# Performance work log

Measured on AMD Instinct MI355X. Metric: run time of the kernel, lower is better.

## Reference

```python
import jax, jax.numpy as jnp
import numpy as np

NUM_LAYERS = 2


def setup_inputs() -> dict:
    key = jax.random.key(0)
    k1, k2, k3, k4 = jax.random.split(key, 4)
    N, E, D = 50000, 800000, 100
    features = jax.random.normal(k1, (N, D), dtype=jnp.float32)
    # stacked nn.Linear weights, one [D,D] per layer (no bias)
    W = jax.random.normal(k2, (NUM_LAYERS, D, D), dtype=jnp.float32) * 0.02
    src = jax.random.randint(k3, (E,), 0, N)
    dst = jax.random.randint(k4, (E,), 0, N)
    return {"features": features, "W": W, "src": src, "dst": dst}


def reference(features, W, src, dst):
    N, D = features.shape
    num_layers = W.shape[0]
    inv_lp1 = 1.0 / (num_layers + 1)

    # --- graph preprocessing (mirrors ItemConv.graph setter) ---
    # add self loops (fill_diag 1.0), then row-normalize by inverse degree
    loop = jnp.arange(N)
    src_all = jnp.concatenate([src, loop])  # message sources
    dst_all = jnp.concatenate([dst, loop])  # message destinations (rows of adj_t)
    deg = jax.ops.segment_sum(
        jnp.ones(src_all.shape, dtype=features.dtype), dst_all, num_segments=N
    )
    deg_inv = jnp.where(deg > 0, 1.0 / deg, 0.0)
    w = deg_inv[dst_all]  # per-edge weight: row-normalized, [E+N]

    # --- forward (LightGCN-style conv with linear projections) ---
    avg = features * inv_lp1
    x = features
    for i in range(num_layers):
        x = x @ W[i].T  # nn.Linear(D, D, bias=False)
        # SpMM: out[d] = sum_{e: dst=d} w_e * x[src_e]
        x = jax.ops.segment_sum(w[:, None] * x[src_all], dst_all, num_segments=N)
        # F.normalize(x): L2 along dim=-1 with eps=1e-12 (max-clamped norm)
        norm = jnp.linalg.norm(x, axis=-1, keepdims=True)
        avg = avg + (x / jnp.maximum(norm, 1e-12)) * inv_lp1
    return avg
```

## Files before the change

kernel.cpp:

```cpp
#include <hip/hip_runtime.h>

#define D 100
#define YSTRIDE 128
#define BSHIFT 7
#define BSIZE 128
#define BMASK 127
#define NBKMAX 512
#define EPB 2048
#define DCAP 4096

typedef __attribute__((ext_vector_type(8))) short bf8v;
typedef __attribute__((ext_vector_type(4))) float f4v;

__device__ inline unsigned short f2bf(float f) {
    unsigned u = __float_as_uint(f);
    return (unsigned short)((u + 0x7fffu + ((u >> 16) & 1u)) >> 16);
}
__device__ inline float bflo(unsigned v) { return __uint_as_float(v << 16); }
__device__ inline float bfhi(unsigned v) { return __uint_as_float(v & 0xffff0000u); }
__device__ inline unsigned short pk8(float a, float b) {
    return (unsigned short)(__builtin_amdgcn_cvt_pk_fp8_f32(a, b, 0, false) & 0xffff);
}
__device__ inline float up8lo(unsigned v) { return __builtin_amdgcn_cvt_f32_fp8((int)v, 0); }
__device__ inline float up8hi(unsigned v) { return __builtin_amdgcn_cvt_f32_fp8((int)v, 1); }

__device__ inline void acc8(float* acc, uint2 v, float w) {
    acc[0] = fmaf(__builtin_amdgcn_cvt_f32_fp8((int)v.x, 0), w, acc[0]);
    acc[1] = fmaf(__builtin_amdgcn_cvt_f32_fp8((int)v.x, 1), w, acc[1]);
    acc[2] = fmaf(__builtin_amdgcn_cvt_f32_fp8((int)v.x, 2), w, acc[2]);
    acc[3] = fmaf(__builtin_amdgcn_cvt_f32_fp8((int)v.x, 3), w, acc[3]);
    acc[4] = fmaf(__builtin_amdgcn_cvt_f32_fp8((int)v.y, 0), w, acc[4]);
    acc[5] = fmaf(__builtin_amdgcn_cvt_f32_fp8((int)v.y, 1), w, acc[5]);
    acc[6] = fmaf(__builtin_amdgcn_cvt_f32_fp8((int)v.y, 2), w, acc[6]);
    acc[7] = fmaf(__builtin_amdgcn_cvt_f32_fp8((int)v.y, 3), w, acc[7]);
}

__device__ inline void scan512_excl(int* a, int* t, int tid) {
    int v0 = a[2 * tid], v1 = a[2 * tid + 1];
    t[tid] = v0 + v1;
    __syncthreads();
    for (int off = 1; off < 256; off <<= 1) {
        int u = (tid >= off) ? t[tid - off] : 0;
        __syncthreads();
        t[tid] += u;
        __syncthreads();
    }
    int base = (tid ? t[tid - 1] : 0);
    a[2 * tid]     = base;
    a[2 * tid + 1] = base + v0;
    __syncthreads();
}

__global__ __launch_bounds__(256) void k_pre(const float* __restrict__ x0, const float* __restrict__ W,
                                             unsigned* __restrict__ s8, float* __restrict__ Wc,
                                             int* __restrict__ hist, const int* __restrict__ dst,
                                             int N, int E, int nbk, int packb, int ablk) {
    __shared__ int lhist[NBKMAX];
    int tid = threadIdx.x;
    int bx = blockIdx.x;

    if (bx < packb) {
        int t = bx * 256 + tid;
        if (t >= N * 32) return;
        int d = t >> 5, q = t & 31;
        unsigned p = 0u;
        if (q < D / 4) {
            float4 v = *(const float4*)(x0 + (long)d * D + q * 4);
            p = (unsigned)pk8(v.x, v.y) | ((unsigned)pk8(v.z, v.w) << 16);
        }
        s8[t] = p;
    } else if (bx < packb + ablk) {
        int blk = bx - packb;
        int base = blk * EPB;
        int count = min(EPB, E - base);
        for (int i = tid; i < NBKMAX; i += 256) lhist[i] = 0;
        __syncthreads();
        for (int i = tid; i < count; i += 256) atomicAdd(&lhist[dst[base + i] >> BSHIFT], 1);
        __syncthreads();
        for (int b = tid; b < NBKMAX; b += 256) hist[(long)blk * NBKMAX + b] = lhist[b];
    } else {
        int t = (bx - packb - ablk) * 256 + tid;
        if (t >= D * D) return;
        int i = t / D, j = t - i * D;
        const float* w2 = W + D * D + (long)i * D;
        float s = 0.f;
        for (int k = 0; k < D; k++) s += w2[k] * W[(long)k * D + j];
        Wc[t] = s;
    }
}

__global__ __launch_bounds__(256) void k_colscan_prep(const int* __restrict__ hist,
                                                      int* __restrict__ pref, int* __restrict__ bcnt,
                                                      int nebk, int nbk,
                                                      const float* __restrict__ W1,
                                                      const float* __restrict__ Wc,
                                                      unsigned short* __restrict__ P, int wtot) {
    int tid = threadIdx.x;
    if ((int)blockIdx.x < nbk) {
        int b = blockIdx.x;
        __shared__ int a[NBKMAX], t[256];
        int i0 = tid, i1 = tid + 256;
        a[i0] = (i0 < nebk) ? hist[(long)i0 * NBKMAX + b] : 0;
        a[i1] = (i1 < nebk) ? hist[(long)i1 * NBKMAX + b] : 0;
        __syncthreads();
        scan512_excl(a, t, tid);
        if (i0 < nebk) pref[(long)i0 * NBKMAX + b] = a[i0];
        if (i1 < nebk) pref[(long)i1 * NBKMAX + b] = a[i1];
        if (tid == 0) bcnt[b] = a[nebk];
    } else {
        int t2 = ((int)blockIdx.x - nbk) * 256 + tid;
        if (t2 >= wtot) return;
        int lane = t2 & 63;
        int r = t2 >> 6;
        int kt = r & 3;
        int r2 = r >> 2;
        int nt = r2 % 7;
        int l  = r2 / 7;
        const float* M = (l == 0) ? W1 : Wc;
        int ng = nt * 16 + (lane & 15);
        int k0 = kt * 32 + (lane >> 4) * 8;
        unsigned short u[8];
#pragma unroll
        for (int j = 0; j < 8; j++) {
            int k = k0 + j;
            u[j] = (ng < D && k < D) ? f2bf(M[(long)ng * D + k]) : (unsigned short)0;
        }
        uint4 o;
        o.x = (unsigned)u[0] | ((unsigned)u[1] << 16);
        o.y = (unsigned)u[2] | ((unsigned)u[3] << 16);
        o.z = (unsigned)u[4] | ((unsigned)u[5] << 16);
        o.w = (unsigned)u[6] | ((unsigned)u[7] << 16);
        *(uint4*)(P + (long)t2 * 8) = o;
    }
}

__global__ __launch_bounds__(256) void k_scanB(const int* __restrict__ bcnt,
                                               int* __restrict__ boff, int nbk, int E) {
    __shared__ int a[NBKMAX], t[256];
    int tid = threadIdx.x;
    a[tid]       = (tid < nbk) ? bcnt[tid] : 0;
    a[tid + 256] = (tid + 256 < nbk) ? bcnt[tid + 256] : 0;
    __syncthreads();
    scan512_excl(a, t, tid);
    if (tid < nbk)       boff[tid] = a[tid];
    if (tid + 256 < nbk) boff[tid + 256] = a[tid + 256];
    if (tid == 0) boff[nbk] = E;
}

__global__ __launch_bounds__(256) void k_bucketC(const int* __restrict__ src,
                                                 const int* __restrict__ dst,
                                                 const int* __restrict__ boff,
                                                 const int* __restrict__ pref,
                                                 unsigned* __restrict__ ebuf, int E, int nbk) {
    __shared__ int lhist[NBKMAX], lstart[NBKMAX], runS[NBKMAX], t[256];
    __shared__ unsigned stage[EPB];
    int tid = threadIdx.x;
    int base = blockIdx.x * EPB;
    int count = min(EPB, E - base);

    for (int i = tid; i < NBKMAX; i += 256) lhist[i] = 0;
    __syncthreads();
    for (int i = tid; i < count; i += 256) atomicAdd(&lhist[dst[base + i] >> BSHIFT], 1);
    __syncthreads();
    for (int i = tid; i < NBKMAX; i += 256) lstart[i] = lhist[i];
    __syncthreads();
    scan512_excl(lstart, t, tid);
    for (int b = tid; b < nbk; b += 256)
        runS[b] = boff[b] + pref[(long)blockIdx.x * NBKMAX + b];
    __syncthreads();
    for (int i = tid; i < NBKMAX; i += 256) lhist[i] = 0;
    __syncthreads();
    for (int i = tid; i < count; i += 256) {
        int dv = dst[base + i];
        int sv = src[base + i];
        int b = dv >> BSHIFT;
        int r = atomicAdd(&lhist[b], 1);
        stage[lstart[b] + r] = ((unsigned)(dv & BMASK) << 16) | (unsigned)sv;
    }
    __syncthreads();
    int wave = tid >> 6, lane = tid & 63;
    for (int b = wave; b < nbk; b += 4) {
        int c = lhist[b], ls = lstart[b], rs = runS[b];
        for (int j = lane; j < c; j += 64) ebuf[rs + j] = stage[ls + j];
    }
}

__global__ __launch_bounds__(256) void k_bucketD(const unsigned* __restrict__ ebuf,
                                                 const int* __restrict__ bucket_off,
                                                 int* __restrict__ col, int* __restrict__ rowptr,
                                                 int N, int nbk, int E) {
    __shared__ int lh[BSIZE], ls[BSIZE];
    __shared__ int colStage[DCAP];
    int b = blockIdx.x;
    int tid = threadIdx.x;
    int beg = bucket_off[b], end = bucket_off[b + 1];
    int cnt = end - beg;

    if (tid < BSIZE) lh[tid] = 0;
    __syncthreads();
    for (int i = tid; i < cnt; i += 256) atomicAdd(&lh[ebuf[beg + i] >> 16], 1);
    __syncthreads();
    if (tid < BSIZE) ls[tid] = lh[tid];
    __syncthreads();
    for (int off = 1; off < BSIZE; off <<= 1) {
        int v = (tid >= off && tid < BSIZE) ? ls[tid - off] : 0;
        __syncthreads();
        if (tid < BSIZE) ls[tid] += v;
        __syncthreads();
    }
    if (tid < BSIZE) ls[tid] -= lh[tid];
    __syncthreads();
    int d0 = b * BSIZE;
    if (tid < BSIZE && d0 + tid < N) rowptr[d0 + tid] = beg + ls[tid];
    if (b == nbk - 1 && tid == 0) rowptr[N] = E;
    if (tid < BSIZE) lh[tid] = 0;
    __syncthreads();
    if (cnt <= DCAP) {
        for (int i = tid; i < cnt; i += 256) {
            unsigned p = ebuf[beg + i];
            int r = p >> 16, s = (int)(p & 0xffffu);
            int k = atomicAdd(&lh[r], 1);
            colStage[ls[r] + k] = s;
        }
        __syncthreads();
        for (int i = tid; i < cnt; i += 256) col[beg + i] = colStage[i];
    } else {
        for (int i = tid; i < cnt; i += 256) {
            unsigned p = ebuf[beg + i];
            int r = p >> 16, s = (int)(p & 0xffffu);
            int k = atomicAdd(&lh[r], 1);
            col[beg + ls[r] + k] = s;
        }
    }
}

__global__ __launch_bounds__(256) void k_spmm(const unsigned short* __restrict__ g8,
                                              const int* __restrict__ rowptr,
                                              const int* __restrict__ col,
                                              const unsigned* __restrict__ self16,
                                              unsigned short* __restrict__ o8,
                                              unsigned* __restrict__ o16,
                                              int write8, int N) {
    int wave = threadIdx.x >> 6;
    int lane = threadIdx.x & 63;
    int g = lane >> 4;
    int j = lane & 15;
    int d = blockIdx.x * 4 + wave;
    if (d >= N) return;

    int b0 = __builtin_amdgcn_readfirstlane(rowptr[d]);
    int e0 = __builtin_amdgcn_readfirstlane(rowptr[d + 1]);

    float acc[8];
    if (g == 0) {
        if (self16) {
            uint4 sv = *((const uint4*)(self16 + (long)d * 64) + j);
            acc[0] = bflo(sv.x); acc[1] = bfhi(sv.x);
            acc[2] = bflo(sv.y); acc[3] = bfhi(sv.y);
            acc[4] = bflo(sv.z); acc[5] = bfhi(sv.z);
            acc[6] = bflo(sv.w); acc[7] = bfhi(sv.w);
        } else {
            uint2 sv = *(const uint2*)(g8 + (long)d * 64 + j * 4);
#pragma unroll
            for (int k = 0; k < 8; k++) acc[k] = 0.f;
            acc8(acc, sv, 1.f);
        }
    } else {
#pragma unroll
        for (int k = 0; k < 8; k++) acc[k] = 0.f;
    }

    for (int win = b0; win < e0; win += 64) {
        int m = e0 - win;
        if (m > 64) m = 64;
        int c = col[win + lane];
        int t = 0;
        for (; t + 8 <= m; t += 8) {
            int sa = __shfl(c, t + g);
            int sb = __shfl(c, t + 4 + g);
            uint2 va = *(const uint2*)(g8 + (long)sa * 64 + j * 4);
            uint2 vb = *(const uint2*)(g8 + (long)sb * 64 + j * 4);
            acc8(acc, va, 1.f);
            acc8(acc, vb, 1.f);
        }
        for (; t < m; t += 4) {
            int rem = m - t;
            int idx = t + ((g < rem) ? g : 0);
            int sa = __shfl(c, idx);
            float w = (g < rem) ? 1.f : 0.f;
            uint2 va = *(const uint2*)(g8 + (long)sa * 64 + j * 4);
            acc8(acc, va, w);
        }
    }

#pragma unroll
    for (int k = 0; k < 8; k++) {
        acc[k] += __shfl_xor(acc[k], 16);
        acc[k] += __shfl_xor(acc[k], 32);
    }

    float dinv = 1.f / (float)(e0 - b0 + 1);
    float r[8];
#pragma unroll
    for (int k = 0; k < 8; k++) r[k] = acc[k] * dinv;

    if (g == 0) {
        uint4 o;
        o.x = (unsigned)f2bf(r[0]) | ((unsigned)f2bf(r[1]) << 16);
        o.y = (unsigned)f2bf(r[2]) | ((unsigned)f2bf(r[3]) << 16);
        o.z = (unsigned)f2bf(r[4]) | ((unsigned)f2bf(r[5]) << 16);
        o.w = (unsigned)f2bf(r[6]) | ((unsigned)f2bf(r[7]) << 16);
        *((uint4*)(o16 + (long)d * 64) + j) = o;
    }
    if (write8 && g == 1) {
        uint2 p;
        p.x = (unsigned)pk8(r[0], r[1]) | ((unsigned)pk8(r[2], r[3]) << 16);
        p.y = (unsigned)pk8(r[4], r[5]) | ((unsigned)pk8(r[6], r[7]) << 16);
        *((uint2*)((unsigned*)o8 + (long)d * 32) + j) = p;
    }
}

__global__ __launch_bounds__(256) void k_epi(const unsigned short* __restrict__ u16,
                                             const unsigned short* __restrict__ v16,
                                             const unsigned short* __restrict__ P,
                                             const float* __restrict__ x0,
                                             float invlp1, float* __restrict__ out, int N) {
    int wave = threadIdx.x >> 6;
    int lane = threadIdx.x & 63;
    int quad = lane >> 4;
    int l16  = lane & 15;
    int rowbase = (blockIdx.x * 4 + wave) * 16;
    if (rowbase >= N) return;
    int arow = rowbase + l16;
    if (arow >= N) arow = N - 1;

    bf8v aU[4], aV[4];
    const unsigned short* ur = u16 + (long)arow * YSTRIDE;
    const unsigned short* vr = v16 + (long)arow * YSTRIDE;
#pragma unroll
    for (int kt = 0; kt < 4; kt++) {
        int k0 = kt * 32 + quad * 8;
        union { bf8v v; uint4 u; } a, b;
        a.u = *(const uint4*)(ur + k0);
        b.u = *(const uint4*)(vr + k0);
        aU[kt] = a.v;
        aV[kt] = b.v;
    }

    f4v accU[7], accV[7];
#pragma unroll
    for (int nt = 0; nt < 7; nt++) { accU[nt] = (f4v){0,0,0,0}; accV[nt] = (f4v){0,0,0,0}; }

    const uint4* bp = (const uint4*)P;
#pragma unroll
    for (int nt = 0; nt < 7; nt++) {
#pragma unroll
        for (int kt = 0; kt < 4; kt++) {
            union { uint4 u; bf8v v; } b1, b2;
            b1.u = bp[(nt * 4 + kt) * 64 + lane];
            b2.u = bp[(28 + nt * 4 + kt) * 64 + lane];
            accU[nt] = __builtin_amdgcn_mfma_f32_16x16x32_bf16(aU[kt], b1.v, accU[nt], 0, 0, 0);
            accV[nt] = __builtin_amdgcn_mfma_f32_16x16x32_bf16(aV[kt], b2.v, accV[nt], 0, 0, 0);
        }
    }

    float sU[4], sV[4];
#pragma unroll
    for (int i = 0; i < 4; i++) {
        float nu = 0.f, nv = 0.f;
#pragma unroll
        for (int nt = 0; nt < 7; nt++) {
            nu += accU[nt][i] * accU[nt][i];
            nv += accV[nt][i] * accV[nt][i];
        }
#pragma unroll
        for (int m = 1; m < 16; m <<= 1) {
            nu += __shfl_xor(nu, m);
            nv += __shfl_xor(nv, m);
        }
        sU[i] = invlp1 / fmaxf(sqrtf(nu), 1e-12f);
        sV[i] = invlp1 / fmaxf(sqrtf(nv), 1e-12f);
    }

#pragma unroll
    for (int nt = 0; nt < 7; nt++) {
        int cc = nt * 16 + l16;
        if (cc < D) {
#pragma unroll
            for (int i = 0; i < 4; i++) {
                int rr = rowbase + quad * 4 + i;
                if (rr < N) {
                    long idx = (long)rr * D + cc;
                    out[idx] = x0[idx] * invlp1 + accU[nt][i] * sU[i] + accV[nt][i] * sV[i];
                }
            }
        }
    }
}


extern "C" void kernel_launch(void* const* d_in, const int* in_sizes, int n_in,
                              void* d_out, int out_size, void* d_ws, size_t ws_size,
                              hipStream_t stream) {
    const float* features = (const float*)d_in[0];
    const float* W        = (const float*)d_in[1];
    const int*   src      = (const int*)d_in[2];
    const int*   dstv     = (const int*)d_in[3];

    int N = in_sizes[0] / D;
    int E = in_sizes[2];
    int L = in_sizes[1] / (D * D);
    float invlp1 = 1.f / (float)(L + 1);
    int NBK = (N + BSIZE - 1) >> BSHIFT;
    int nebk = (E + EPB - 1) / EPB;

    char*  ws  = (char*)d_ws;
    size_t off = 0;
    auto alloc = [&](size_t bytes) -> void* {
        void* p = (void*)(ws + off);
        off += (bytes + 255) & ~(size_t)255;
        return p;
    };
    unsigned*       s8     = (unsigned*)alloc((size_t)N * 32 * sizeof(unsigned));
    unsigned*       u8     = (unsigned*)alloc((size_t)N * 32 * sizeof(unsigned));
    unsigned*       u16    = (unsigned*)alloc((size_t)N * 64 * sizeof(unsigned));
    unsigned*       v16    = (unsigned*)alloc((size_t)N * 64 * sizeof(unsigned));
    float*          Wc     = (float*)alloc((size_t)D * D * sizeof(float));
    unsigned short* wpack  = (unsigned short*)alloc((size_t)2 * 7 * 4 * 64 * 8 * sizeof(unsigned short));
    unsigned*       ebuf   = (unsigned*)alloc((size_t)E * sizeof(unsigned));
    int*            colb   = (int*)alloc((size_t)E * sizeof(int));
    int*            rowptr = (int*)alloc((size_t)(N + 1) * sizeof(int));
    int*            hist   = (int*)alloc((size_t)nebk * NBKMAX * sizeof(int));
    int*            pref   = (int*)alloc((size_t)nebk * NBKMAX * sizeof(int));
    int*            bcnt   = (int*)alloc((size_t)NBKMAX * sizeof(int));
    int*            boff   = (int*)alloc((size_t)(NBKMAX + 1) * sizeof(int));

    int wtot  = 2 * 7 * 4 * 64;
    int packb = (N * 32 + 255) / 256;
    int wcb   = (D * D + 255) / 256;
    int prepb = (wtot + 255) / 256;

    k_pre<<<packb + nebk + wcb, 256, 0, stream>>>(features, W, s8, Wc, hist, dstv,
                                                  N, E, NBK, packb, nebk);
    k_colscan_prep<<<NBK + prepb, 256, 0, stream>>>(hist, pref, bcnt, nebk, NBK,
                                                    W, Wc, wpack, wtot);
    k_scanB<<<1, 256, 0, stream>>>(bcnt, boff, NBK, E);
    k_bucketC<<<nebk, 256, 0, stream>>>(src, dstv, boff, pref, ebuf, E, NBK);
    k_bucketD<<<NBK, 256, 0, stream>>>(ebuf, boff, colb, rowptr, N, NBK, E);

    int spmmblocks = (N + 3) / 4;
    k_spmm<<<spmmblocks, 256, 0, stream>>>((const unsigned short*)s8, rowptr, colb,
                                           (const unsigned*)nullptr,
                                           (unsigned short*)u8, u16, 1, N);
    k_spmm<<<spmmblocks, 256, 0, stream>>>((const unsigned short*)u8, rowptr, colb,
                                           u16, (unsigned short*)nullptr, v16, 0, N);

    int nrowtiles = (N + 15) / 16;
    int epiblocks = (nrowtiles + 3) / 4;
    k_epi<<<epiblocks, 256, 0, stream>>>((const unsigned short*)u16, (const unsigned short*)v16,
                                         wpack, features, invlp1, (float*)d_out, N);
}
```

Before: 200.5 us.

## Fuse all pipeline stages into one cooperative persistent kernel with grid syncs

Replaces the eight separate kernel launches (preprocessing, scans, bucketing, two SpMM passes, epilogue) with one cooperative kernel. The stages are separated by grid-wide barriers and use grid-stride loops over a persistent grid sized from occupancy. The goal is to remove per-launch overhead and inter-kernel gaps. The risks are lower occupancy, because the single kernel carries the register and shared-memory footprint of its heaviest stage, and the cost of each grid.sync. The global bucket-offset scan is now recomputed redundantly in every bucketing block instead of running as a separate kernel.

```diff
diff --git a/kernel.cpp b/kernel.cpp
--- a/kernel.cpp
+++ b/kernel.cpp
@@ -1,4 +1,7 @@
 #include <hip/hip_runtime.h>
+#include <hip/hip_cooperative_groups.h>
+
+namespace cg = cooperative_groups;
 
 #define D 100
 #define YSTRIDE 128
@@ -8,6 +11,8 @@
 #define NBKMAX 512
 #define EPB 2048
 #define DCAP 4096
+#define WTOT (2 * 7 * 4 * 64)
+#define WCB 40
 
 typedef __attribute__((ext_vector_type(8))) short bf8v;
 typedef __attribute__((ext_vector_type(4))) float f4v;
@@ -21,8 +26,6 @@
 __device__ inline unsigned short pk8(float a, float b) {
     return (unsigned short)(__builtin_amdgcn_cvt_pk_fp8_f32(a, b, 0, false) & 0xffff);
 }
-__device__ inline float up8lo(unsigned v) { return __builtin_amdgcn_cvt_f32_fp8((int)v, 0); }
-__device__ inline float up8hi(unsigned v) { return __builtin_amdgcn_cvt_f32_fp8((int)v, 1); }
 
 __device__ inline void acc8(float* acc, uint2 v, float w) {
     acc[0] = fmaf(__builtin_amdgcn_cvt_f32_fp8((int)v.x, 0), w, acc[0]);
@@ -51,203 +54,13 @@
     __syncthreads();
 }
 
-__global__ __launch_bounds__(256) void k_pre(const float* __restrict__ x0, const float* __restrict__ W,
-                                             unsigned* __restrict__ s8, float* __restrict__ Wc,
-                                             int* __restrict__ hist, const int* __restrict__ dst,
-                                             int N, int E, int nbk, int packb, int ablk) {
-    __shared__ int lhist[NBKMAX];
-    int tid = threadIdx.x;
-    int bx = blockIdx.x;
-
-    if (bx < packb) {
-        int t = bx * 256 + tid;
-        if (t >= N * 32) return;
-        int d = t >> 5, q = t & 31;
-        unsigned p = 0u;
-        if (q < D / 4) {
-            float4 v = *(const float4*)(x0 + (long)d * D + q * 4);
-            p = (unsigned)pk8(v.x, v.y) | ((unsigned)pk8(v.z, v.w) << 16);
-        }
-        s8[t] = p;
-    } else if (bx < packb + ablk) {
-        int blk = bx - packb;
-        int base = blk * EPB;
-        int count = min(EPB, E - base);
-        for (int i = tid; i < NBKMAX; i += 256) lhist[i] = 0;
-        __syncthreads();
-        for (int i = tid; i < count; i += 256) atomicAdd(&lhist[dst[base + i] >> BSHIFT], 1);
-        __syncthreads();
-        for (int b = tid; b < NBKMAX; b += 256) hist[(long)blk * NBKMAX + b] = lhist[b];
-    } else {
-        int t = (bx - packb - ablk) * 256 + tid;
-        if (t >= D * D) return;
-        int i = t / D, j = t - i * D;
-        const float* w2 = W + D * D + (long)i * D;
-        float s = 0.f;
-        for (int k = 0; k < D; k++) s += w2[k] * W[(long)k * D + j];
-        Wc[t] = s;
-    }
-}
-
-__global__ __launch_bounds__(256) void k_colscan_prep(const int* __restrict__ hist,
-                                                      int* __restrict__ pref, int* __restrict__ bcnt,
-                                                      int nebk, int nbk,
-                                                      const float* __restrict__ W1,
-                                                      const float* __restrict__ Wc,
-                                                      unsigned short* __restrict__ P, int wtot) {
-    int tid = threadIdx.x;
-    if ((int)blockIdx.x < nbk) {
-        int b = blockIdx.x;
-        __shared__ int a[NBKMAX], t[256];
-        int i0 = tid, i1 = tid + 256;
-        a[i0] = (i0 < nebk) ? hist[(long)i0 * NBKMAX + b] : 0;
-        a[i1] = (i1 < nebk) ? hist[(long)i1 * NBKMAX + b] : 0;
-        __syncthreads();
-        scan512_excl(a, t, tid);
-        if (i0 < nebk) pref[(long)i0 * NBKMAX + b] = a[i0];
-        if (i1 < nebk) pref[(long)i1 * NBKMAX + b] = a[i1];
-        if (tid == 0) bcnt[b] = a[nebk];
-    } else {
-        int t2 = ((int)blockIdx.x - nbk) * 256 + tid;
-        if (t2 >= wtot) return;
-        int lane = t2 & 63;
-        int r = t2 >> 6;
-        int kt = r & 3;
-        int r2 = r >> 2;
-        int nt = r2 % 7;
-        int l  = r2 / 7;
-        const float* M = (l == 0) ? W1 : Wc;
-        int ng = nt * 16 + (lane & 15);
-        int k0 = kt * 32 + (lane >> 4) * 8;
-        unsigned short u[8];
-#pragma unroll
-        for (int j = 0; j < 8; j++) {
-            int k = k0 + j;
-            u[j] = (ng < D && k < D) ? f2bf(M[(long)ng * D + k]) : (unsigned short)0;
-        }
-        uint4 o;
-        o.x = (unsigned)u[0] | ((unsigned)u[1] << 16);
-        o.y = (unsigned)u[2] | ((unsigned)u[3] << 16);
-        o.z = (unsigned)u[4] | ((unsigned)u[5] << 16);
-        o.w = (unsigned)u[6] | ((unsigned)u[7] << 16);
-        *(uint4*)(P + (long)t2 * 8) = o;
-    }
-}
-
-__global__ __launch_bounds__(256) void k_scanB(const int* __restrict__ bcnt,
-                                               int* __restrict__ boff, int nbk, int E) {
-    __shared__ int a[NBKMAX], t[256];
-    int tid = threadIdx.x;
-    a[tid]       = (tid < nbk) ? bcnt[tid] : 0;
-    a[tid + 256] = (tid + 256 < nbk) ? bcnt[tid + 256] : 0;
-    __syncthreads();
-    scan512_excl(a, t, tid);
-    if (tid < nbk)       boff[tid] = a[tid];
-    if (tid + 256 < nbk) boff[tid + 256] = a[tid + 256];
-    if (tid == 0) boff[nbk] = E;
-}
-
-__global__ __launch_bounds__(256) void k_bucketC(const int* __restrict__ src,
-                                                 const int* __restrict__ dst,
-                                                 const int* __restrict__ boff,
-                                                 const int* __restrict__ pref,
-                                                 unsigned* __restrict__ ebuf, int E, int nbk) {
-    __shared__ int lhist[NBKMAX], lstart[NBKMAX], runS[NBKMAX], t[256];
-    __shared__ unsigned stage[EPB];
-    int tid = threadIdx.x;
-    int base = blockIdx.x * EPB;
-    int count = min(EPB, E - base);
-
-    for (int i = tid; i < NBKMAX; i += 256) lhist[i] = 0;
-    __syncthreads();
-    for (int i = tid; i < count; i += 256) atomicAdd(&lhist[dst[base + i] >> BSHIFT], 1);
-    __syncthreads();
-    for (int i = tid; i < NBKMAX; i += 256) lstart[i] = lhist[i];
-    __syncthreads();
-    scan512_excl(lstart, t, tid);
-    for (int b = tid; b < nbk; b += 256)
-        runS[b] = boff[b] + pref[(long)blockIdx.x * NBKMAX + b];
-    __syncthreads();
-    for (int i = tid; i < NBKMAX; i += 256) lhist[i] = 0;
-    __syncthreads();
-    for (int i = tid; i < count; i += 256) {
-        int dv = dst[base + i];
-        int sv = src[base + i];
-        int b = dv >> BSHIFT;
-        int r = atomicAdd(&lhist[b], 1);
-        stage[lstart[b] + r] = ((unsigned)(dv & BMASK) << 16) | (unsigned)sv;
-    }
-    __syncthreads();
-    int wave = tid >> 6, lane = tid & 63;
-    for (int b = wave; b < nbk; b += 4) {
-        int c = lhist[b], ls = lstart[b], rs = runS[b];
-        for (int j = lane; j < c; j += 64) ebuf[rs + j] = stage[ls + j];
-    }
-}
-
-__global__ __launch_bounds__(256) void k_bucketD(const unsigned* __restrict__ ebuf,
-                                                 const int* __restrict__ bucket_off,
-                                                 int* __restrict__ col, int* __restrict__ rowptr,
-                                                 int N, int nbk, int E) {
-    __shared__ int lh[BSIZE], ls[BSIZE];
-    __shared__ int colStage[DCAP];
-    int b = blockIdx.x;
-    int tid = threadIdx.x;
-    int beg = bucket_off[b], end = bucket_off[b + 1];
-    int cnt = end - beg;
-
-    if (tid < BSIZE) lh[tid] = 0;
-    __syncthreads();
-    for (int i = tid; i < cnt; i += 256) atomicAdd(&lh[ebuf[beg + i] >> 16], 1);
-    __syncthreads();
-    if (tid < BSIZE) ls[tid] = lh[tid];
-    __syncthreads();
-    for (int off = 1; off < BSIZE; off <<= 1) {
-        int v = (tid >= off && tid < BSIZE) ? ls[tid - off] : 0;
-        __syncthreads();
-        if (tid < BSIZE) ls[tid] += v;
-        __syncthreads();
-    }
-    if (tid < BSIZE) ls[tid] -= lh[tid];
-    __syncthreads();
-    int d0 = b * BSIZE;
-    if (tid < BSIZE && d0 + tid < N) rowptr[d0 + tid] = beg + ls[tid];
-    if (b == nbk - 1 && tid == 0) rowptr[N] = E;
-    if (tid < BSIZE) lh[tid] = 0;
-    __syncthreads();
-    if (cnt <= DCAP) {
-        for (int i = tid; i < cnt; i += 256) {
-            unsigned p = ebuf[beg + i];
-            int r = p >> 16, s = (int)(p & 0xffffu);
-            int k = atomicAdd(&lh[r], 1);
-            colStage[ls[r] + k] = s;
-        }
-        __syncthreads();
-        for (int i = tid; i < cnt; i += 256) col[beg + i] = colStage[i];
-    } else {
-        for (int i = tid; i < cnt; i += 256) {
-            unsigned p = ebuf[beg + i];
-            int r = p >> 16, s = (int)(p & 0xffffu);
-            int k = atomicAdd(&lh[r], 1);
-            col[beg + ls[r] + k] = s;
-        }
-    }
-}
-
-__global__ __launch_bounds__(256) void k_spmm(const unsigned short* __restrict__ g8,
-                                              const int* __restrict__ rowptr,
-                                              const int* __restrict__ col,
-                                              const unsigned* __restrict__ self16,
-                                              unsigned short* __restrict__ o8,
-                                              unsigned* __restrict__ o16,
-                                              int write8, int N) {
-    int wave = threadIdx.x >> 6;
-    int lane = threadIdx.x & 63;
-    int g = lane >> 4;
-    int j = lane & 15;
-    int d = blockIdx.x * 4 + wave;
-    if (d >= N) return;
-
+__device__ inline void spmm_node(const unsigned short* __restrict__ g8,
+                                 const int* __restrict__ rowptr,
+                                 const int* __restrict__ col,
+                                 const unsigned* __restrict__ self16,
+                                 unsigned* __restrict__ o8,
+                                 unsigned* __restrict__ o16,
+                                 int write8, int d, int lane, int g, int j) {
     int b0 = __builtin_amdgcn_readfirstlane(rowptr[d]);
     int e0 = __builtin_amdgcn_readfirstlane(rowptr[d + 1]);
 
@@ -316,82 +129,295 @@
         uint2 p;
         p.x = (unsigned)pk8(r[0], r[1]) | ((unsigned)pk8(r[2], r[3]) << 16);
         p.y = (unsigned)pk8(r[4], r[5]) | ((unsigned)pk8(r[6], r[7]) << 16);
-        *((uint2*)((unsigned*)o8 + (long)d * 32) + j) = p;
-    }
-}
-
-__global__ __launch_bounds__(256) void k_epi(const unsigned short* __restrict__ u16,
-                                             const unsigned short* __restrict__ v16,
-                                             const unsigned short* __restrict__ P,
-                                             const float* __restrict__ x0,
-                                             float invlp1, float* __restrict__ out, int N) {
-    int wave = threadIdx.x >> 6;
-    int lane = threadIdx.x & 63;
-    int quad = lane >> 4;
-    int l16  = lane & 15;
-    int rowbase = (blockIdx.x * 4 + wave) * 16;
-    if (rowbase >= N) return;
-    int arow = rowbase + l16;
-    if (arow >= N) arow = N - 1;
-
-    bf8v aU[4], aV[4];
-    const unsigned short* ur = u16 + (long)arow * YSTRIDE;
-    const unsigned short* vr = v16 + (long)arow * YSTRIDE;
-#pragma unroll
-    for (int kt = 0; kt < 4; kt++) {
-        int k0 = kt * 32 + quad * 8;
-        union { bf8v v; uint4 u; } a, b;
-        a.u = *(const uint4*)(ur + k0);
-        b.u = *(const uint4*)(vr + k0);
-        aU[kt] = a.v;
-        aV[kt] = b.v;
-    }
-
-    f4v accU[7], accV[7];
-#pragma unroll
-    for (int nt = 0; nt < 7; nt++) { accU[nt] = (f4v){0,0,0,0}; accV[nt] = (f4v){0,0,0,0}; }
-
-    const uint4* bp = (const uint4*)P;
-#pragma unroll
-    for (int nt = 0; nt < 7; nt++) {
-#pragma unroll
-        for (int kt = 0; kt < 4; kt++) {
-            union { uint4 u; bf8v v; } b1, b2;
-            b1.u = bp[(nt * 4 + kt) * 64 + lane];
-            b2.u = bp[(28 + nt * 4 + kt) * 64 + lane];
-            accU[nt] = __builtin_amdgcn_mfma_f32_16x16x32_bf16(aU[kt], b1.v, accU[nt], 0, 0, 0);
-            accV[nt] = __builtin_amdgcn_mfma_f32_16x16x32_bf16(aV[kt], b2.v, accV[nt], 0, 0, 0);
-        }
-    }
-
-    float sU[4], sV[4];
-#pragma unroll
-    for (int i = 0; i < 4; i++) {
-        float nu = 0.f, nv = 0.f;
-#pragma unroll
-        for (int nt = 0; nt < 7; nt++) {
-            nu += accU[nt][i] * accU[nt][i];
-            nv += accV[nt][i] * accV[nt][i];
-        }
-#pragma unroll
-        for (int m = 1; m < 16; m <<= 1) {
-            nu += __shfl_xor(nu, m);
-            nv += __shfl_xor(nv, m);
-        }
-        sU[i] = invlp1 / fmaxf(sqrtf(nu), 1e-12f);
-        sV[i] = invlp1 / fmaxf(sqrtf(nv), 1e-12f);
-    }
-
-#pragma unroll
-    for (int nt = 0; nt < 7; nt++) {
-        int cc = nt * 16 + l16;
-        if (cc < D) {
+        *((uint2*)(o8 + (long)d * 32) + j) = p;
+    }
+}
+
+__global__ void mega(const float* __restrict__ x0, const float* __restrict__ W,
+                     const int* __restrict__ srcv, const int* __restrict__ dstv,
+                     unsigned* __restrict__ s8, unsigned* __restrict__ u8,
+                     unsigned* __restrict__ u16, unsigned* __restrict__ v16,
+                     float* __restrict__ Wc, unsigned short* __restrict__ wpack,
+                     unsigned* __restrict__ ebuf, int* __restrict__ colb,
+                     int* __restrict__ rowptr,
+                     int* __restrict__ hist, int* __restrict__ pref, int* __restrict__ bcnt,
+                     float invlp1, float* __restrict__ out,
+                     int N, int E, int nbk, int nebk, int packB, int prepb) {
+    __shared__ __align__(16) char smem_raw[20480];
+    int tid = threadIdx.x;
+    cg::grid_group grid = cg::this_grid();
+
+    {
+        int bx = blockIdx.x;
+        if (bx < packB) {
+            for (int t = bx * 256 + tid; t < N * 32; t += packB * 256) {
+                int d = t >> 5, q = t & 31;
+                unsigned p = 0u;
+                if (q < D / 4) {
+                    float4 v = *(const float4*)(x0 + (long)d * D + q * 4);
+                    p = (unsigned)pk8(v.x, v.y) | ((unsigned)pk8(v.z, v.w) << 16);
+                }
+                s8[t] = p;
+            }
+        } else if (bx < packB + nebk) {
+            int blk = bx - packB;
+            int* lhist = (int*)smem_raw;
+            int base = blk * EPB;
+            int count = min(EPB, E - base);
+            for (int i = tid; i < NBKMAX; i += 256) lhist[i] = 0;
+            __syncthreads();
+            for (int i = tid; i < count; i += 256) atomicAdd(&lhist[dstv[base + i] >> BSHIFT], 1);
+            __syncthreads();
+            for (int b = tid; b < NBKMAX; b += 256) hist[(long)blk * NBKMAX + b] = lhist[b];
+        } else {
+            int t = (bx - packB - nebk) * 256 + tid;
+            if (t < D * D) {
+                int i = t / D, j = t - i * D;
+                const float* w2 = W + D * D + (long)i * D;
+                float s = 0.f;
+                for (int k = 0; k < D; k++) s += w2[k] * W[(long)k * D + j];
+                Wc[t] = s;
+            }
+        }
+    }
+    grid.sync();
+
+    for (int w = blockIdx.x; w < nbk + prepb; w += gridDim.x) {
+        if (w < nbk) {
+            int b = w;
+            int* a = (int*)smem_raw;
+            int* t2 = a + 512;
+            int i0 = tid, i1 = tid + 256;
+            a[i0] = (i0 < nebk) ? hist[(long)i0 * NBKMAX + b] : 0;
+            a[i1] = (i1 < nebk) ? hist[(long)i1 * NBKMAX + b] : 0;
+            __syncthreads();
+            scan512_excl(a, t2, tid);
+            if (i0 < nebk) pref[(long)i0 * NBKMAX + b] = a[i0];
+            if (i1 < nebk) pref[(long)i1 * NBKMAX + b] = a[i1];
+            if (tid == 0) bcnt[b] = a[nebk];
+        } else {
+            int t2 = (w - nbk) * 256 + tid;
+            if (t2 < WTOT) {
+                int lane = t2 & 63;
+                int r = t2 >> 6;
+                int kt = r & 3;
+                int r2 = r >> 2;
+                int nt = r2 % 7;
+                int l  = r2 / 7;
+                const float* M = (l == 0) ? W : Wc;
+                int ng = nt * 16 + (lane & 15);
+                int k0 = kt * 32 + (lane >> 4) * 8;
+                unsigned short u[8];
+#pragma unroll
+                for (int j = 0; j < 8; j++) {
+                    int k = k0 + j;
+                    u[j] = (ng < D && k < D) ? f2bf(M[(long)ng * D + k]) : (unsigned short)0;
+                }
+                uint4 o;
+                o.x = (unsigned)u[0] | ((unsigned)u[1] << 16);
+                o.y = (unsigned)u[2] | ((unsigned)u[3] << 16);
+                o.z = (unsigned)u[4] | ((unsigned)u[5] << 16);
+                o.w = (unsigned)u[6] | ((unsigned)u[7] << 16);
+                *(uint4*)(wpack + (long)t2 * 8) = o;
+            }
+        }
+        __syncthreads();
+    }
+    grid.sync();
+
+    for (int ch = blockIdx.x; ch < nebk; ch += gridDim.x) {
+        int* bscan  = (int*)smem_raw;
+        int* lhist  = bscan + 512;
+        int* lstart = lhist + 512;
+        int* runS   = lstart + 512;
+        int* t2     = runS + 512;
+        unsigned* stage = (unsigned*)(t2 + 256);
+        int base = ch * EPB;
+        int count = min(EPB, E - base);
+
+        bscan[tid]       = (tid < nbk) ? bcnt[tid] : 0;
+        bscan[tid + 256] = (tid + 256 < nbk) ? bcnt[tid + 256] : 0;
+        __syncthreads();
+        scan512_excl(bscan, t2, tid);
+
+        for (int i = tid; i < NBKMAX; i += 256) lhist[i] = 0;
+        __syncthreads();
+        for (int i = tid; i < count; i += 256) atomicAdd(&lhist[dstv[base + i] >> BSHIFT], 1);
+        __syncthreads();
+        for (int i = tid; i < NBKMAX; i += 256) lstart[i] = lhist[i];
+        __syncthreads();
+        scan512_excl(lstart, t2, tid);
+        for (int b = tid; b < nbk; b += 256)
+            runS[b] = bscan[b] + pref[(long)ch * NBKMAX + b];
+        __syncthreads();
+        for (int i = tid; i < NBKMAX; i += 256) lhist[i] = 0;
+        __syncthreads();
+        for (int i = tid; i < count; i += 256) {
+            int dv = dstv[base + i];
+            int sv = srcv[base + i];
+            int b = dv >> BSHIFT;
+            int r = atomicAdd(&lhist[b], 1);
+            stage[lstart[b] + r] = ((unsigned)(dv & BMASK) << 16) | (unsigned)sv;
+        }
+        __syncthreads();
+        int wave = tid >> 6, lane = tid & 63;
+        for (int b = wave; b < nbk; b += 4) {
+            int c = lhist[b], ls2 = lstart[b], rs = runS[b];
+            for (int j2 = lane; j2 < c; j2 += 64) ebuf[rs + j2] = stage[ls2 + j2];
+        }
+        __syncthreads();
+    }
+    grid.sync();
+
+    for (int b = blockIdx.x; b < nbk; b += gridDim.x) {
+        int* bscan = (int*)smem_raw;
+        int* t2 = bscan + 512;
+        int* lh = t2 + 256;
+        int* ls = lh + 128;
+        int* colStage = ls + 128;
+
+        bscan[tid]       = (tid < nbk) ? bcnt[tid] : 0;
+        bscan[tid + 256] = (tid + 256 < nbk) ? bcnt[tid + 256] : 0;
+        __syncthreads();
+        scan512_excl(bscan, t2, tid);
+        int beg = bscan[b];
+        int end = bscan[b + 1];
+        int cnt = end - beg;
+
+        if (tid < BSIZE) lh[tid] = 0;
+        __syncthreads();
+        for (int i = tid; i < cnt; i += 256) atomicAdd(&lh[ebuf[beg + i] >> 16], 1);
+        __syncthreads();
+        if (tid < BSIZE) ls[tid] = lh[tid];
+        __syncthreads();
+        for (int off = 1; off < BSIZE; off <<= 1) {
+            int v = (tid >= off && tid < BSIZE) ? ls[tid - off] : 0;
+            __syncthreads();
+            if (tid < BSIZE) ls[tid] += v;
+            __syncthreads();
+        }
+        if (tid < BSIZE) ls[tid] -= lh[tid];
+        __syncthreads();
+        int d0 = b * BSIZE;
+        if (tid < BSIZE && d0 + tid < N) rowptr[d0 + tid] = beg + ls[tid];
+        if (b == nbk - 1 && tid == 0) rowptr[N] = E;
+        if (tid < BSIZE) lh[tid] = 0;
+        __syncthreads();
+        if (cnt <= DCAP) {
+            for (int i = tid; i < cnt; i += 256) {
+                unsigned p = ebuf[beg + i];
+                int r = p >> 16, s = (int)(p & 0xffffu);
+                int k = atomicAdd(&lh[r], 1);
+                colStage[ls[r] + k] = s;
+            }
+            __syncthreads();
+            for (int i = tid; i < cnt; i += 256) colb[beg + i] = colStage[i];
+        } else {
+            for (int i = tid; i < cnt; i += 256) {
+                unsigned p = ebuf[beg + i];
+                int r = p >> 16, s = (int)(p & 0xffffu);
+                int k = atomicAdd(&lh[r], 1);
+                colb[beg + ls[r] + k] = s;
+            }
+        }
+        __syncthreads();
+    }
+    grid.sync();
+
+    {
+        int lane = tid & 63, g = lane >> 4, j = lane & 15;
+        int wid = blockIdx.x * 4 + (tid >> 6);
+        int nw = gridDim.x * 4;
+        for (int d = wid; d < N; d += nw)
+            spmm_node((const unsigned short*)s8, rowptr, colb, (const unsigned*)0,
+                      u8, u16, 1, d, lane, g, j);
+    }
+    grid.sync();
+
+    {
+        int lane = tid & 63, g = lane >> 4, j = lane & 15;
+        int wid = blockIdx.x * 4 + (tid >> 6);
+        int nw = gridDim.x * 4;
+        for (int d = wid; d < N; d += nw)
+            spmm_node((const unsigned short*)u8, rowptr, colb, u16,
+                      (unsigned*)0, v16, 0, d, lane, g, j);
+    }
+    grid.sync();
+
+    {
+        int lane = tid & 63;
+        int quad = lane >> 4;
+        int l16  = lane & 15;
+        int wid = blockIdx.x * 4 + (tid >> 6);
+        int nw = gridDim.x * 4;
+        int ntiles = (N + 15) / 16;
+        const unsigned short* u16s = (const unsigned short*)u16;
+        const unsigned short* v16s = (const unsigned short*)v16;
+        const uint4* bp = (const uint4*)wpack;
+        for (int tile = wid; tile < ntiles; tile += nw) {
+            int rowbase = tile * 16;
+            int arow = rowbase + l16;
+            if (arow >= N) arow = N - 1;
+
+            bf8v aU[4], aV[4];
+            const unsigned short* ur = u16s + (long)arow * YSTRIDE;
+            const unsigned short* vr = v16s + (long)arow * YSTRIDE;
+#pragma unroll
+            for (int kt = 0; kt < 4; kt++) {
+                int k0 = kt * 32 + quad * 8;
+                union { bf8v v; uint4 u; } a, b;
+                a.u = *(const uint4*)(ur + k0);
+                b.u = *(const uint4*)(vr + k0);
+                aU[kt] = a.v;
+                aV[kt] = b.v;
+            }
+
+            f4v accU[7], accV[7];
+#pragma unroll
+            for (int nt = 0; nt < 7; nt++) { accU[nt] = (f4v){0,0,0,0}; accV[nt] = (f4v){0,0,0,0}; }
+
+#pragma unroll
+            for (int nt = 0; nt < 7; nt++) {
+#pragma unroll
+                for (int kt = 0; kt < 4; kt++) {
+                    union { uint4 u; bf8v v; } b1, b2;
+                    b1.u = bp[(nt * 4 + kt) * 64 + lane];
+                    b2.u = bp[(28 + nt * 4 + kt) * 64 + lane];
+                    accU[nt] = __builtin_amdgcn_mfma_f32_16x16x32_bf16(aU[kt], b1.v, accU[nt], 0, 0, 0);
+                    accV[nt] = __builtin_amdgcn_mfma_f32_16x16x32_bf16(aV[kt], b2.v, accV[nt], 0, 0, 0);
+                }
+            }
+
+            float sU[4], sV[4];
 #pragma unroll
             for (int i = 0; i < 4; i++) {
-                int rr = rowbase + quad * 4 + i;
-                if (rr < N) {
-                    long idx = (long)rr * D + cc;
-                    out[idx] = x0[idx] * invlp1 + accU[nt][i] * sU[i] + accV[nt][i] * sV[i];
+                float nu = 0.f, nv = 0.f;
+#pragma unroll
+                for (int nt = 0; nt < 7; nt++) {
+                    nu += accU[nt][i] * accU[nt][i];
+                    nv += accV[nt][i] * accV[nt][i];
+                }
+#pragma unroll
+                for (int m = 1; m < 16; m <<= 1) {
+                    nu += __shfl_xor(nu, m);
+                    nv += __shfl_xor(nv, m);
+                }
+                sU[i] = invlp1 / fmaxf(sqrtf(nu), 1e-12f);
+                sV[i] = invlp1 / fmaxf(sqrtf(nv), 1e-12f);
+            }
+
+#pragma unroll
+            for (int nt = 0; nt < 7; nt++) {
+                int cc = nt * 16 + l16;
+                if (cc < D) {
+#pragma unroll
+                    for (int i = 0; i < 4; i++) {
+                        int rr = rowbase + quad * 4 + i;
+                        if (rr < N) {
+                            long idx = (long)rr * D + cc;
+                            out[idx] = x0[idx] * invlp1 + accU[nt][i] * sU[i] + accV[nt][i] * sV[i];
+                        }
+                    }
                 }
             }
         }
@@ -426,37 +452,38 @@
     unsigned*       u16    = (unsigned*)alloc((size_t)N * 64 * sizeof(unsigned));
     unsigned*       v16    = (unsigned*)alloc((size_t)N * 64 * sizeof(unsigned));
     float*          Wc     = (float*)alloc((size_t)D * D * sizeof(float));
-    unsigned short* wpack  = (unsigned short*)alloc((size_t)2 * 7 * 4 * 64 * 8 * sizeof(unsigned short));
+    unsigned short* wpack  = (unsigned short*)alloc((size_t)WTOT * 8 * sizeof(unsigned short));
     unsigned*       ebuf   = (unsigned*)alloc((size_t)E * sizeof(unsigned));
     int*            colb   = (int*)alloc((size_t)E * sizeof(int));
     int*            rowptr = (int*)alloc((size_t)(N + 1) * sizeof(int));
     int*            hist   = (int*)alloc((size_t)nebk * NBKMAX * sizeof(int));
     int*            pref   = (int*)alloc((size_t)nebk * NBKMAX * sizeof(int));
     int*            bcnt   = (int*)alloc((size_t)NBKMAX * sizeof(int));
-    int*            boff   = (int*)alloc((size_t)(NBKMAX + 1) * sizeof(int));
-
-    int wtot  = 2 * 7 * 4 * 64;
-    int packb = (N * 32 + 255) / 256;
-    int wcb   = (D * D + 255) / 256;
-    int prepb = (wtot + 255) / 256;
-
-    k_pre<<<packb + nebk + wcb, 256, 0, stream>>>(features, W, s8, Wc, hist, dstv,
-                                                  N, E, NBK, packb, nebk);
-    k_colscan_prep<<<NBK + prepb, 256, 0, stream>>>(hist, pref, bcnt, nebk, NBK,
-                                                    W, Wc, wpack, wtot);
-    k_scanB<<<1, 256, 0, stream>>>(bcnt, boff, NBK, E);
-    k_bucketC<<<nebk, 256, 0, stream>>>(src, dstv, boff, pref, ebuf, E, NBK);
-    k_bucketD<<<NBK, 256, 0, stream>>>(ebuf, boff, colb, rowptr, N, NBK, E);
-
-    int spmmblocks = (N + 3) / 4;
-    k_spmm<<<spmmblocks, 256, 0, stream>>>((const unsigned short*)s8, rowptr, colb,
-                                           (const unsigned*)nullptr,
-                                           (unsigned short*)u8, u16, 1, N);
-    k_spmm<<<spmmblocks, 256, 0, stream>>>((const unsigned short*)u8, rowptr, colb,
-                                           u16, (unsigned short*)nullptr, v16, 0, N);
-
-    int nrowtiles = (N + 15) / 16;
-    int epiblocks = (nrowtiles + 3) / 4;
-    k_epi<<<epiblocks, 256, 0, stream>>>((const unsigned short*)u16, (const unsigned short*)v16,
-                                         wpack, features, invlp1, (float*)d_out, N);
-}
+
+    int prepb = (WTOT + 255) / 256;
+
+    static int G = 0;
+    if (G == 0) {
+        int maxB = 0;
+        hipOccupancyMaxActiveBlocksPerMultiprocessor(&maxB, (const void*)mega, 256, 0);
+        int nCU = 0;
+        hipDeviceGetAttribute(&nCU, hipDeviceAttributeMultiprocessorCount, 0);
+        if (maxB < 1) maxB = 1;
+        if (nCU < 1) nCU = 256;
+        G = maxB * nCU;
+        if (G > 2048) G = 2048;
+        if (G < nebk + WCB + 1) G = nebk + WCB + 1;
+    }
+    int packB = G - nebk - WCB;
+
+    float* outp = (float*)d_out;
+    void* args[] = {
+        (void*)&features, (void*)&W, (void*)&src, (void*)&dstv,
+        (void*)&s8, (void*)&u8, (void*)&u16, (void*)&v16,
+        (void*)&Wc, (void*)&wpack, (void*)&ebuf, (void*)&colb, (void*)&rowptr,
+        (void*)&hist, (void*)&pref, (void*)&bcnt,
+        (void*)&invlp1, (void*)&outp,
+        (void*)&N, (void*)&E, (void*)&NBK, (void*)&nebk, (void*)&packB, (void*)&prepb
+    };
+    hipLaunchCooperativeKernel((const void*)mega, dim3(G), dim3(256), args, 0, stream);
+}
```

New measurement: 686.6 us. 3.42x slower.
